# Kernel tuning notes

Hardware: AMD Instinct MI355X
Metric: run time of the kernel (lower is better)

The kernel has to match this reference:

```python
import jax, jax.numpy as jnp
import numpy as np

ENCODER_DIM, DECODER_DIM, ATTENTION_DIM = 2048, 512, 512
B, P = 128, 196  # batch, num_pixels


def setup_inputs() -> dict:
    key = jax.random.key(0)
    ks = jax.random.split(key, 8)
    s_e = 1.0 / np.sqrt(ENCODER_DIM)
    s_d = 1.0 / np.sqrt(DECODER_DIM)
    s_a = 1.0 / np.sqrt(ATTENTION_DIM)
    return {
        "encoder_out": jax.random.normal(ks[0], (B, P, ENCODER_DIM), jnp.float32),
        "decoder_hidden": jax.random.normal(ks[1], (B, DECODER_DIM), jnp.float32),
        "W_enc": jax.random.uniform(ks[2], (ENCODER_DIM, ATTENTION_DIM), jnp.float32, -s_e, s_e),
        "b_enc": jax.random.uniform(ks[3], (ATTENTION_DIM,), jnp.float32, -s_e, s_e),
        "W_dec": jax.random.uniform(ks[4], (DECODER_DIM, ATTENTION_DIM), jnp.float32, -s_d, s_d),
        "b_dec": jax.random.uniform(ks[5], (ATTENTION_DIM,), jnp.float32, -s_d, s_d),
        "W_full": jax.random.uniform(ks[6], (ATTENTION_DIM,), jnp.float32, -s_a, s_a),
        "b_full": jax.random.uniform(ks[7], (), jnp.float32, -s_a, s_a),
    }


def reference(encoder_out, decoder_hidden, W_enc, b_enc, W_dec, b_dec, W_full, b_full):
    # att1: [B, P, A]; att2: [B, A]
    att1 = jnp.einsum('bpe,ea->bpa', encoder_out, W_enc) + b_enc
    att2 = jnp.einsum('bd,da->ba', decoder_hidden, W_dec) + b_dec
    # broadcast add over pixel dim, relu, linear-to-scalar -> [B, P]
    att = jnp.einsum('bpa,a->bp', jax.nn.relu(att1 + att2[:, None, :]), W_full) + b_full
    alpha = jax.nn.softmax(att, axis=1)  # softmax over pixels
    attention_weighted_encoding = jnp.einsum('bpe,bp->be', encoder_out, alpha)
    return attention_weighted_encoding, alpha
```

## Files before the change

kernel.cpp:

```cpp
#include <hip/hip_runtime.h>
#include <hip/hip_bf16.h>

#define BATCH 128
#define PIX   196
#define EDIM  2048
#define DDIM  512
#define ADIM  512
#define MTOT  (BATCH*PIX)
#define BK    32
#define NK    (EDIM/BK)

typedef __attribute__((ext_vector_type(8))) short short8;
typedef __attribute__((ext_vector_type(4))) float f32x4;

__device__ __forceinline__ unsigned short f2bf(float f) {
    union { float f; unsigned int u; } c; c.f = f;
    unsigned int u = c.u;
    u += 0x7fffu + ((u >> 16) & 1u);
    return (unsigned short)(u >> 16);
}

__device__ __forceinline__ short8 cvt8(float4 a, float4 b) {
    short8 v;
    v[0] = (short)f2bf(a.x); v[1] = (short)f2bf(a.y);
    v[2] = (short)f2bf(a.z); v[3] = (short)f2bf(a.w);
    v[4] = (short)f2bf(b.x); v[5] = (short)f2bf(b.y);
    v[6] = (short)f2bf(b.z); v[7] = (short)f2bf(b.w);
    return v;
}

#define GLOAD16(gp, lp) __builtin_amdgcn_global_load_lds( \
    (const __attribute__((address_space(1))) void*)(gp),  \
    (__attribute__((address_space(3))) void*)(lp), 16, 0, 0)

#define MFMA16(a, b, c) __builtin_amdgcn_mfma_f32_16x16x32_bf16(a, b, c, 0, 0, 0)

__global__ __launch_bounds__(256) void pack_wenc(const float* __restrict__ Wenc,
                                                 unsigned short* __restrict__ WTp) {
    __shared__ float f[32 * ADIM];
    const int kt = blockIdx.x;
    const int tid = threadIdx.x;
    const float4* src = (const float4*)(Wenc + (size_t)kt * 32 * ADIM);
    float4* dst = (float4*)f;
    #pragma unroll
    for (int i = 0; i < 16; ++i)
        dst[tid + i * 256] = src[tid + i * 256];
    __syncthreads();
    for (int c = tid; c < 2048; c += 256) {
        int n  = ((c >> 6) << 4) + ((c >> 2) & 15);
        int kc = c & 3;
        short8 v;
        #pragma unroll
        for (int d = 0; d < 8; ++d)
            v[d] = (short)f2bf(f[(kc * 8 + d) * ADIM + n]);
        *(short8*)(WTp + (size_t)kt * 16384 + (size_t)c * 8) = v;
    }
}

__global__ __launch_bounds__(256) void bias_kernel(const float* __restrict__ dec,
                                                   const float* __restrict__ Wdec,
                                                   const float* __restrict__ b_enc,
                                                   const float* __restrict__ b_dec,
                                                   float* __restrict__ bias) {
    __shared__ float ds[4 * DDIM];
    const int b0 = blockIdx.x * 4;
    for (int i = threadIdx.x; i < 4 * DDIM; i += 256)
        ds[i] = dec[(size_t)b0 * DDIM + i];
    __syncthreads();
    const int a0 = threadIdx.x * 2;
    float acc0[4] = {0.f, 0.f, 0.f, 0.f};
    float acc1[4] = {0.f, 0.f, 0.f, 0.f};
    for (int d = 0; d < DDIM; d++) {
        float2 w = *(const float2*)&Wdec[(size_t)d * ADIM + a0];
        #pragma unroll
        for (int bi = 0; bi < 4; bi++) {
            float dv = ds[bi * DDIM + d];
            acc0[bi] += dv * w.x;
            acc1[bi] += dv * w.y;
        }
    }
    float be0 = b_enc[a0] + b_dec[a0];
    float be1 = b_enc[a0 + 1] + b_dec[a0 + 1];
    #pragma unroll
    for (int bi = 0; bi < 4; bi++) {
        bias[(size_t)(b0 + bi) * ADIM + a0]     = acc0[bi] + be0;
        bias[(size_t)(b0 + bi) * ADIM + a0 + 1] = acc1[bi] + be1;
    }
}

__global__ __launch_bounds__(512, 2) void gemm_att(const float* __restrict__ enc,
                                                   const unsigned short* __restrict__ WTp,
                                                   const float* __restrict__ bias,
                                                   const float* __restrict__ Wfull,
                                                   float* __restrict__ att) {
    __shared__ __align__(16) char ldsA[2][8192];
    __shared__ __align__(16) char ldsB[3][32768];
    __shared__ float red[4][128];

    const int tid  = threadIdx.x;
    const int lane = tid & 63;
    const int wid  = tid >> 6;
    const int wm   = wid >> 2;
    const int wn   = wid & 3;
    const int cif  = lane & 15;
    const int rgrp = lane >> 4;
    const int loff = cif * 64 + rgrp * 16;
    const int m0   = blockIdx.x * 128;

    const float* pA = enc + (size_t)(m0 + (tid >> 2)) * EDIM + (tid & 3) * 8;
    const unsigned aWoff = (unsigned)(wid * 1024 + lane * 16);
    const char* pB = (const char*)WTp + (size_t)wid * 4096 + (size_t)lane * 16;
    const unsigned bgOff = (unsigned)(wid * 4096);

    char* aR = ldsA[0]; char* aW = ldsA[1];
    char* bR = ldsB[0]; char* bN1 = ldsB[1]; char* bN2 = ldsB[2];

    f32x4 acc[4][8] = {};
    float4 rg[2][2];

    float4 t0 = *(const float4*)pA;
    float4 t1 = *(const float4*)(pA + 4);
    rg[1][0] = *(const float4*)(pA + BK);
    rg[1][1] = *(const float4*)(pA + BK + 4);
    #pragma unroll
    for (int c = 0; c < 4; ++c)
        GLOAD16(pB + c * 1024, bR + bgOff + c * 1024);
    #pragma unroll
    for (int c = 0; c < 4; ++c)
        GLOAD16(pB + 32768 + c * 1024, bN1 + bgOff + c * 1024);
    *(short8*)(aR + aWoff) = cvt8(t0, t1);
    asm volatile("s_waitcnt vmcnt(4)" ::: "memory");
    asm volatile("s_waitcnt lgkmcnt(0)" ::: "memory");
    __builtin_amdgcn_s_barrier();

    #pragma unroll 2
    for (int kt = 0; kt < NK - 2; ++kt) {
        const char* ps = pB + (size_t)(kt + 2) * 32768;
        #pragma unroll
        for (int c = 0; c < 4; ++c)
            GLOAD16(ps + c * 1024, bN2 + bgOff + c * 1024);
        {
            const float* pa = pA + (kt + 2) * BK;
            rg[kt & 1][0] = *(const float4*)pa;
            rg[kt & 1][1] = *(const float4*)(pa + 4);
        }
        {
            short8 a[4], b[8];
            #pragma unroll
            for (int i = 0; i < 4; ++i)
                a[i] = *(const short8*)(aR + (wm * 4 + i) * 1024 + loff);
            #pragma unroll
            for (int j = 0; j < 8; ++j)
                b[j] = *(const short8*)(bR + (wn * 8 + j) * 1024 + loff);
            __builtin_amdgcn_s_setprio(1);
            #pragma unroll
            for (int i = 0; i < 4; ++i)
                #pragma unroll
                for (int j = 0; j < 8; ++j)
                    acc[i][j] = MFMA16(a[i], b[j], acc[i][j]);
            __builtin_amdgcn_s_setprio(0);
        }
        *(short8*)(aW + aWoff) = cvt8(rg[(kt + 1) & 1][0], rg[(kt + 1) & 1][1]);
        asm volatile("s_waitcnt vmcnt(6)" ::: "memory");
        asm volatile("s_waitcnt lgkmcnt(0)" ::: "memory");
        __builtin_amdgcn_s_barrier();
        { char* t = bR; bR = bN1; bN1 = bN2; bN2 = t; }
        { char* t = aR; aR = aW; aW = t; }
    }

    {
        short8 a[4], b[8];
        #pragma unroll
        for (int i = 0; i < 4; ++i)
            a[i] = *(const short8*)(aR + (wm * 4 + i) * 1024 + loff);
        #pragma unroll
        for (int j = 0; j < 8; ++j)
            b[j] = *(const short8*)(bR + (wn * 8 + j) * 1024 + loff);
        __builtin_amdgcn_s_setprio(1);
        #pragma unroll
        for (int i = 0; i < 4; ++i)
            #pragma unroll
            for (int j = 0; j < 8; ++j)
                acc[i][j] = MFMA16(a[i], b[j], acc[i][j]);
        __builtin_amdgcn_s_setprio(0);
        *(short8*)(aW + aWoff) = cvt8(rg[(NK - 1) & 1][0], rg[(NK - 1) & 1][1]);
        asm volatile("s_waitcnt vmcnt(0)" ::: "memory");
        asm volatile("s_waitcnt lgkmcnt(0)" ::: "memory");
        __builtin_amdgcn_s_barrier();
        { char* t = bR; bR = bN1; bN1 = bN2; bN2 = t; }
        { char* t = aR; aR = aW; aW = t; }
    }
    {
        short8 a[4], b[8];
        #pragma unroll
        for (int i = 0; i < 4; ++i)
            a[i] = *(const short8*)(aR + (wm * 4 + i) * 1024 + loff);
        #pragma unroll
        for (int j = 0; j < 8; ++j)
            b[j] = *(const short8*)(bR + (wn * 8 + j) * 1024 + loff);
        #pragma unroll
        for (int i = 0; i < 4; ++i)
            #pragma unroll
            for (int j = 0; j < 8; ++j)
                acc[i][j] = MFMA16(a[i], b[j], acc[i][j]);
    }

    const int bf  = m0 / PIX;
    const int thr = (bf + 1) * PIX;
    const int bfc = (bf + 1 < BATCH) ? bf + 1 : BATCH - 1;
    float wf[8], bs0[8], bs1[8];
    #pragma unroll
    for (int j = 0; j < 8; ++j) {
        int aj = wn * 128 + j * 16 + cif;
        wf[j]  = Wfull[aj];
        bs0[j] = bias[(size_t)bf  * ADIM + aj];
        bs1[j] = bias[(size_t)bfc * ADIM + aj];
    }
    #pragma unroll
    for (int i = 0; i < 4; ++i) {
        #pragma unroll
        for (int r = 0; r < 4; ++r) {
            int ml = wm * 64 + i * 16 + rgrp * 4 + r;
            int m  = m0 + ml;
            bool sec = (m >= thr);
            float s = 0.f;
            #pragma unroll
            for (int j = 0; j < 8; ++j) {
                float v = acc[i][j][r] + (sec ? bs1[j] : bs0[j]);
                s += fmaxf(v, 0.f) * wf[j];
            }
            s += __shfl_xor(s, 1);
            s += __shfl_xor(s, 2);
            s += __shfl_xor(s, 4);
            s += __shfl_xor(s, 8);
            if (cif == 0) red[wn][ml] = s;
        }
    }
    __syncthreads();
    if (tid < 128)
        att[m0 + tid] = red[0][tid] + red[1][tid] + red[2][tid] + red[3][tid];
}

__global__ __launch_bounds__(256) void softmax_kernel(const float* __restrict__ att,
                                                      float* __restrict__ alpha) {
    const int b = blockIdx.x;
    const int tid = threadIdx.x;
    const int lane = tid & 63, wid = tid >> 6;
    __shared__ float wred[4];

    float x = (tid < PIX) ? att[(size_t)b * PIX + tid] : -1e30f;
    float m = x;
    #pragma unroll
    for (int off = 32; off >= 1; off >>= 1) m = fmaxf(m, __shfl_xor(m, off));
    if (lane == 0) wred[wid] = m;
    __syncthreads();
    float gm = fmaxf(fmaxf(wred[0], wred[1]), fmaxf(wred[2], wred[3]));
    __syncthreads();

    float e = (tid < PIX) ? __expf(x - gm) : 0.f;
    float s = e;
    #pragma unroll
    for (int off = 32; off >= 1; off >>= 1) s += __shfl_xor(s, off);
    if (lane == 0) wred[wid] = s;
    __syncthreads();
    float gs = wred[0] + wred[1] + wred[2] + wred[3];

    if (tid < PIX) alpha[(size_t)b * PIX + tid] = e / gs;
}

__global__ __launch_bounds__(128) void weighted_kernel(const float* __restrict__ enc,
                                                       const float* __restrict__ alpha,
                                                       float* __restrict__ out) {
    const int b = blockIdx.x >> 2;
    const int q = blockIdx.x & 3;
    const int tid = threadIdx.x;
    __shared__ float al[PIX];
    for (int i = tid; i < PIX; i += 128) al[i] = alpha[(size_t)b * PIX + i];
    __syncthreads();

    const int e = q * 512 + tid * 4;
    const float4* src = (const float4*)(enc + (size_t)b * PIX * EDIM + e);
    float ax = 0.f, ay = 0.f, az = 0.f, aw = 0.f;
    #pragma unroll 4
    for (int p = 0; p < PIX; p++) {
        float av = al[p];
        float4 v = src[(size_t)p * (EDIM / 4)];
        ax += av * v.x; ay += av * v.y; az += av * v.z; aw += av * v.w;
    }
    float4 o; o.x = ax; o.y = ay; o.z = az; o.w = aw;
    *(float4*)&out[(size_t)b * EDIM + e] = o;
}

extern "C" void kernel_launch(void* const* d_in, const int* in_sizes, int n_in,
                              void* d_out, int out_size, void* d_ws, size_t ws_size,
                              hipStream_t stream) {
    const float* enc   = (const float*)d_in[0];
    const float* dec   = (const float*)d_in[1];
    const float* Wenc  = (const float*)d_in[2];
    const float* benc  = (const float*)d_in[3];
    const float* Wdec  = (const float*)d_in[4];
    const float* bdec  = (const float*)d_in[5];
    const float* Wfull = (const float*)d_in[6];

    float* out_awe   = (float*)d_out;
    float* out_alpha = (float*)d_out + BATCH * EDIM;

    char* ws = (char*)d_ws;
    unsigned short* WTp = (unsigned short*)ws;
    float* bias = (float*)(ws + (size_t)ADIM * EDIM * 2);
    float* att  = (float*)(ws + (size_t)ADIM * EDIM * 2 + (size_t)BATCH * ADIM * 4);

    pack_wenc<<<NK, 256, 0, stream>>>(Wenc, WTp);
    bias_kernel<<<BATCH / 4, 256, 0, stream>>>(dec, Wdec, benc, bdec, bias);
    gemm_att<<<MTOT / 128, 512, 0, stream>>>(enc, WTp, bias, Wfull, att);
    softmax_kernel<<<BATCH, 256, 0, stream>>>(att, out_alpha);
    weighted_kernel<<<BATCH * 4, 128, 0, stream>>>(enc, out_alpha, out_awe);
}
```

Before: 132.9 us.

## Split attention GEMM across N-slices with register-resident A and partial sums

The attention GEMM is restructured so each block computes one 128-wide slice of the attention dimension for 128 rows, using 128 threads instead of 512, which gives four times as many blocks. Each wave loads its A rows straight into registers and converts them to bf16 there, so A no longer passes through LDS; only B is staged in double-buffered LDS. The per-slice partial scores go to a workspace and are summed in the softmax kernel. The aim is better occupancy and less LDS traffic, at the cost of each A row being read from global memory four times (once per slice) and extra partial-score writes.

```diff
diff --git a/kernel.cpp b/kernel.cpp
--- a/kernel.cpp
+++ b/kernel.cpp
@@ -9,6 +9,9 @@
 #define MTOT  (BATCH*PIX)
 #define BK    32
 #define NK    (EDIM/BK)
+#define NSLC  4
+#define BN    128
+#define BM    128
 
 typedef __attribute__((ext_vector_type(8))) short short8;
 typedef __attribute__((ext_vector_type(4))) float f32x4;
@@ -22,10 +25,14 @@
 
 __device__ __forceinline__ short8 cvt8(float4 a, float4 b) {
     short8 v;
-    v[0] = (short)f2bf(a.x); v[1] = (short)f2bf(a.y);
-    v[2] = (short)f2bf(a.z); v[3] = (short)f2bf(a.w);
-    v[4] = (short)f2bf(b.x); v[5] = (short)f2bf(b.y);
-    v[6] = (short)f2bf(b.z); v[7] = (short)f2bf(b.w);
+    v[0] = (short)__bfloat16_as_ushort(__float2bfloat16(a.x));
+    v[1] = (short)__bfloat16_as_ushort(__float2bfloat16(a.y));
+    v[2] = (short)__bfloat16_as_ushort(__float2bfloat16(a.z));
+    v[3] = (short)__bfloat16_as_ushort(__float2bfloat16(a.w));
+    v[4] = (short)__bfloat16_as_ushort(__float2bfloat16(b.x));
+    v[5] = (short)__bfloat16_as_ushort(__float2bfloat16(b.y));
+    v[6] = (short)__bfloat16_as_ushort(__float2bfloat16(b.z));
+    v[7] = (short)__bfloat16_as_ushort(__float2bfloat16(b.w));
     return v;
 }
 
@@ -47,8 +54,12 @@
         dst[tid + i * 256] = src[tid + i * 256];
     __syncthreads();
     for (int c = tid; c < 2048; c += 256) {
-        int n  = ((c >> 6) << 4) + ((c >> 2) & 15);
-        int kc = c & 3;
+        int ns   = c >> 9;
+        int cl   = c & 511;
+        int j    = cl >> 6;
+        int nl16 = (cl >> 2) & 15;
+        int kc   = cl & 3;
+        int n    = ns * 128 + j * 16 + nl16;
         short8 v;
         #pragma unroll
         for (int d = 0; d < 8; ++d)
@@ -88,121 +99,99 @@
     }
 }
 
-__global__ __launch_bounds__(512, 2) void gemm_att(const float* __restrict__ enc,
+__global__ __launch_bounds__(128, 2) void gemm_att(const float* __restrict__ enc,
                                                    const unsigned short* __restrict__ WTp,
                                                    const float* __restrict__ bias,
                                                    const float* __restrict__ Wfull,
-                                                   float* __restrict__ att) {
-    __shared__ __align__(16) char ldsA[2][8192];
-    __shared__ __align__(16) char ldsB[3][32768];
-    __shared__ float red[4][128];
+                                                   float* __restrict__ att_part) {
+    __shared__ __align__(16) char ldsB[2][8192];
 
     const int tid  = threadIdx.x;
     const int lane = tid & 63;
     const int wid  = tid >> 6;
-    const int wm   = wid >> 2;
-    const int wn   = wid & 3;
     const int cif  = lane & 15;
     const int rgrp = lane >> 4;
-    const int loff = cif * 64 + rgrp * 16;
-    const int m0   = blockIdx.x * 128;
-
-    const float* pA = enc + (size_t)(m0 + (tid >> 2)) * EDIM + (tid & 3) * 8;
-    const unsigned aWoff = (unsigned)(wid * 1024 + lane * 16);
-    const char* pB = (const char*)WTp + (size_t)wid * 4096 + (size_t)lane * 16;
-    const unsigned bgOff = (unsigned)(wid * 4096);
-
-    char* aR = ldsA[0]; char* aW = ldsA[1];
-    char* bR = ldsB[0]; char* bN1 = ldsB[1]; char* bN2 = ldsB[2];
+    const int bid  = blockIdx.x;
+    const int ns   = bid & 3;
+    const int m0   = (bid >> 2) * BM;
+
+    const char* pB = (const char*)WTp + (size_t)ns * 8192 + (size_t)wid * 4096
+                   + (size_t)lane * 16;
+    const unsigned bOff = (unsigned)(wid * 4096 + lane * 16);
+
+    const float* pA[4];
+    #pragma unroll
+    for (int i = 0; i < 4; ++i)
+        pA[i] = enc + (size_t)(m0 + wid * 64 + i * 16 + cif) * EDIM + rgrp * 8;
+
+    char* bR = ldsB[0];
+    char* bW = ldsB[1];
 
     f32x4 acc[4][8] = {};
-    float4 rg[2][2];
-
-    float4 t0 = *(const float4*)pA;
-    float4 t1 = *(const float4*)(pA + 4);
-    rg[1][0] = *(const float4*)(pA + BK);
-    rg[1][1] = *(const float4*)(pA + BK + 4);
+    float4 areg[8];
+    short8 ac[4];
+
     #pragma unroll
     for (int c = 0; c < 4; ++c)
-        GLOAD16(pB + c * 1024, bR + bgOff + c * 1024);
-    #pragma unroll
-    for (int c = 0; c < 4; ++c)
-        GLOAD16(pB + 32768 + c * 1024, bN1 + bgOff + c * 1024);
-    *(short8*)(aR + aWoff) = cvt8(t0, t1);
-    asm volatile("s_waitcnt vmcnt(4)" ::: "memory");
-    asm volatile("s_waitcnt lgkmcnt(0)" ::: "memory");
+        GLOAD16(pB + c * 1024, bR + bOff + c * 1024);
+    #pragma unroll
+    for (int i = 0; i < 4; ++i) {
+        areg[2 * i]     = *(const float4*)pA[i];
+        areg[2 * i + 1] = *(const float4*)(pA[i] + 4);
+    }
+    asm volatile("s_waitcnt vmcnt(8)" ::: "memory");
     __builtin_amdgcn_s_barrier();
+    __builtin_amdgcn_sched_barrier(0);
 
     #pragma unroll 2
-    for (int kt = 0; kt < NK - 2; ++kt) {
-        const char* ps = pB + (size_t)(kt + 2) * 32768;
+    for (int kt = 0; kt < NK - 1; ++kt) {
+        const char* ps = pB + (size_t)(kt + 1) * 32768;
         #pragma unroll
         for (int c = 0; c < 4; ++c)
-            GLOAD16(ps + c * 1024, bN2 + bgOff + c * 1024);
-        {
-            const float* pa = pA + (kt + 2) * BK;
-            rg[kt & 1][0] = *(const float4*)pa;
-            rg[kt & 1][1] = *(const float4*)(pa + 4);
+            GLOAD16(ps + c * 1024, bW + bOff + c * 1024);
+        asm volatile("s_waitcnt vmcnt(4)" ::: "memory");
+        #pragma unroll
+        for (int i = 0; i < 4; ++i)
+            ac[i] = cvt8(areg[2 * i], areg[2 * i + 1]);
+        #pragma unroll
+        for (int i = 0; i < 4; ++i) {
+            const float* pa = pA[i] + (size_t)(kt + 1) * BK;
+            areg[2 * i]     = *(const float4*)pa;
+            areg[2 * i + 1] = *(const float4*)(pa + 4);
         }
         {
-            short8 a[4], b[8];
-            #pragma unroll
-            for (int i = 0; i < 4; ++i)
-                a[i] = *(const short8*)(aR + (wm * 4 + i) * 1024 + loff);
+            short8 b[8];
             #pragma unroll
             for (int j = 0; j < 8; ++j)
-                b[j] = *(const short8*)(bR + (wn * 8 + j) * 1024 + loff);
+                b[j] = *(const short8*)(bR + j * 1024 + cif * 64 + rgrp * 16);
             __builtin_amdgcn_s_setprio(1);
             #pragma unroll
             for (int i = 0; i < 4; ++i)
                 #pragma unroll
                 for (int j = 0; j < 8; ++j)
-                    acc[i][j] = MFMA16(a[i], b[j], acc[i][j]);
+                    acc[i][j] = MFMA16(ac[i], b[j], acc[i][j]);
             __builtin_amdgcn_s_setprio(0);
         }
-        *(short8*)(aW + aWoff) = cvt8(rg[(kt + 1) & 1][0], rg[(kt + 1) & 1][1]);
-        asm volatile("s_waitcnt vmcnt(6)" ::: "memory");
-        asm volatile("s_waitcnt lgkmcnt(0)" ::: "memory");
+        asm volatile("s_waitcnt vmcnt(8) lgkmcnt(0)" ::: "memory");
         __builtin_amdgcn_s_barrier();
-        { char* t = bR; bR = bN1; bN1 = bN2; bN2 = t; }
-        { char* t = aR; aR = aW; aW = t; }
-    }
-
+        __builtin_amdgcn_sched_barrier(0);
+        { char* t = bR; bR = bW; bW = t; }
+    }
+
+    asm volatile("s_waitcnt vmcnt(0)" ::: "memory");
+    #pragma unroll
+    for (int i = 0; i < 4; ++i)
+        ac[i] = cvt8(areg[2 * i], areg[2 * i + 1]);
     {
-        short8 a[4], b[8];
-        #pragma unroll
-        for (int i = 0; i < 4; ++i)
-            a[i] = *(const short8*)(aR + (wm * 4 + i) * 1024 + loff);
+        short8 b[8];
         #pragma unroll
         for (int j = 0; j < 8; ++j)
-            b[j] = *(const short8*)(bR + (wn * 8 + j) * 1024 + loff);
-        __builtin_amdgcn_s_setprio(1);
+            b[j] = *(const short8*)(bR + j * 1024 + cif * 64 + rgrp * 16);
         #pragma unroll
         for (int i = 0; i < 4; ++i)
             #pragma unroll
             for (int j = 0; j < 8; ++j)
-                acc[i][j] = MFMA16(a[i], b[j], acc[i][j]);
-        __builtin_amdgcn_s_setprio(0);
-        *(short8*)(aW + aWoff) = cvt8(rg[(NK - 1) & 1][0], rg[(NK - 1) & 1][1]);
-        asm volatile("s_waitcnt vmcnt(0)" ::: "memory");
-        asm volatile("s_waitcnt lgkmcnt(0)" ::: "memory");
-        __builtin_amdgcn_s_barrier();
-        { char* t = bR; bR = bN1; bN1 = bN2; bN2 = t; }
-        { char* t = aR; aR = aW; aW = t; }
-    }
-    {
-        short8 a[4], b[8];
-        #pragma unroll
-        for (int i = 0; i < 4; ++i)
-            a[i] = *(const short8*)(aR + (wm * 4 + i) * 1024 + loff);
-        #pragma unroll
-        for (int j = 0; j < 8; ++j)
-            b[j] = *(const short8*)(bR + (wn * 8 + j) * 1024 + loff);
-        #pragma unroll
-        for (int i = 0; i < 4; ++i)
-            #pragma unroll
-            for (int j = 0; j < 8; ++j)
-                acc[i][j] = MFMA16(a[i], b[j], acc[i][j]);
+                acc[i][j] = MFMA16(ac[i], b[j], acc[i][j]);
     }
 
     const int bf  = m0 / PIX;
@@ -211,7 +200,7 @@
     float wf[8], bs0[8], bs1[8];
     #pragma unroll
     for (int j = 0; j < 8; ++j) {
-        int aj = wn * 128 + j * 16 + cif;
+        int aj = ns * 128 + j * 16 + cif;
         wf[j]  = Wfull[aj];
         bs0[j] = bias[(size_t)bf  * ADIM + aj];
         bs1[j] = bias[(size_t)bfc * ADIM + aj];
@@ -220,7 +209,7 @@
     for (int i = 0; i < 4; ++i) {
         #pragma unroll
         for (int r = 0; r < 4; ++r) {
-            int ml = wm * 64 + i * 16 + rgrp * 4 + r;
+            int ml = wid * 64 + i * 16 + rgrp * 4 + r;
             int m  = m0 + ml;
             bool sec = (m >= thr);
             float s = 0.f;
@@ -233,26 +222,28 @@
             s += __shfl_xor(s, 2);
             s += __shfl_xor(s, 4);
             s += __shfl_xor(s, 8);
-            if (cif == 0) red[wn][ml] = s;
+            if (cif == 0) att_part[(size_t)ns * MTOT + m] = s;
         }
     }
-    __syncthreads();
-    if (tid < 128)
-        att[m0 + tid] = red[0][tid] + red[1][tid] + red[2][tid] + red[3][tid];
-}
-
-__global__ __launch_bounds__(256) void softmax_kernel(const float* __restrict__ att,
+}
+
+__global__ __launch_bounds__(256) void softmax_kernel(const float* __restrict__ att_part,
                                                       float* __restrict__ alpha) {
     const int b = blockIdx.x;
     const int tid = threadIdx.x;
     const int lane = tid & 63, wid = tid >> 6;
     __shared__ float wred[4];
 
-    float x = (tid < PIX) ? att[(size_t)b * PIX + tid] : -1e30f;
-    float m = x;
-    #pragma unroll
-    for (int off = 32; off >= 1; off >>= 1) m = fmaxf(m, __shfl_xor(m, off));
-    if (lane == 0) wred[wid] = m;
+    float x = -1e30f;
+    if (tid < PIX) {
+        size_t m = (size_t)b * PIX + tid;
+        x = att_part[m] + att_part[MTOT + m] + att_part[2 * MTOT + m]
+          + att_part[3 * MTOT + m];
+    }
+    float mx = x;
+    #pragma unroll
+    for (int off = 32; off >= 1; off >>= 1) mx = fmaxf(mx, __shfl_xor(mx, off));
+    if (lane == 0) wred[wid] = mx;
     __syncthreads();
     float gm = fmaxf(fmaxf(wred[0], wred[1]), fmaxf(wred[2], wred[3]));
     __syncthreads();
@@ -308,11 +299,12 @@
     char* ws = (char*)d_ws;
     unsigned short* WTp = (unsigned short*)ws;
     float* bias = (float*)(ws + (size_t)ADIM * EDIM * 2);
-    float* att  = (float*)(ws + (size_t)ADIM * EDIM * 2 + (size_t)BATCH * ADIM * 4);
+    float* att_part = (float*)(ws + (size_t)ADIM * EDIM * 2
+                             + (size_t)BATCH * ADIM * 4);
 
     pack_wenc<<<NK, 256, 0, stream>>>(Wenc, WTp);
     bias_kernel<<<BATCH / 4, 256, 0, stream>>>(dec, Wdec, benc, bdec, bias);
-    gemm_att<<<MTOT / 128, 512, 0, stream>>>(enc, WTp, bias, Wfull, att);
-    softmax_kernel<<<BATCH, 256, 0, stream>>>(att, out_alpha);
+    gemm_att<<<(MTOT / BM) * NSLC, 128, 0, stream>>>(enc, WTp, bias, Wfull, att_part);
+    softmax_kernel<<<BATCH, 256, 0, stream>>>(att_part, out_alpha);
     weighted_kernel<<<BATCH * 4, 128, 0, stream>>>(enc, out_alpha, out_awe);
 }
```

Result: slower. 266.4 us, median of 4 (+100.4%).
